# Optimization experiments

Measured on AMD Instinct MI355X. Metric: run time of the kernel, lower is better.

Reference implementation:

```python
import jax, jax.numpy as jnp
import numpy as np

MA_K = 25  # moving-average window for temporal pattern decoupling (trend extraction)
BN_EPS = 1e-5


def conv1d(x, w, b, dilation=1, padding=0, groups=1):
    # x: [N, C, L], w: [O, I/groups, K]
    out = jax.lax.conv_general_dilated(
        x, w, window_strides=(1,), padding=[(padding, padding)],
        rhs_dilation=(dilation,), dimension_numbers=("NCH", "OIH", "NCH"),
        feature_group_count=groups)
    if b is not None:
        out = out + b[None, :, None]
    return out


def moving_avg(x):
    # series-decomposition trend: depthwise uniform conv with edge padding
    c = x.shape[1]
    xp = jnp.pad(x, ((0, 0), (0, 0), (MA_K // 2, MA_K // 2)), mode="edge")
    k = jnp.full((c, 1, MA_K), 1.0 / MA_K, dtype=x.dtype)
    return conv1d(xp, k, None, dilation=1, padding=0, groups=c)


def setup_inputs() -> dict:
    key = jax.random.key(0)
    ks = jax.random.split(key, 12)
    B, C, L = 16, 256, 4096
    nb = 4
    c = C // nb  # 64 per branch
    inp = {
        "x": jax.random.normal(ks[0], (B, C, L), dtype=jnp.float32),
        # stacked per-branch Conv1dBlock params (all branches share c)
        "conv_w": jax.random.normal(ks[1], (nb, c, c, 3), dtype=jnp.float32) * 0.05,
        "conv_b": jax.random.normal(ks[2], (nb, c), dtype=jnp.float32) * 0.05,
        "bn_gamma": 1.0 + 0.1 * jax.random.normal(ks[3], (nb, c), dtype=jnp.float32),
        "bn_beta": 0.1 * jax.random.normal(ks[4], (nb, c), dtype=jnp.float32),
        "bn_mean": 0.1 * jax.random.normal(ks[5], (nb, c), dtype=jnp.float32),
        "bn_var": 0.5 + jax.random.uniform(ks[6], (nb, c), dtype=jnp.float32),
        # fusion 1x1 conv: 2C -> C
        "fusion_w": jax.random.normal(ks[7], (C, 2 * C, 1), dtype=jnp.float32) * 0.02,
        "fusion_b": jax.random.normal(ks[8], (C,), dtype=jnp.float32) * 0.02,
        "alpha": jnp.ones((1,), dtype=jnp.float32),
    }
    return inp


def reference(x, conv_w, conv_b, bn_gamma, bn_beta, bn_mean, bn_var,
              fusion_w, fusion_b, alpha):
    nb = conv_w.shape[0]
    parts = jnp.split(x, nb, axis=1)  # equal branch channels (C % nb == 0)
    shorts, longs = [], []
    for i in range(nb):
        d = 2 ** i  # dilation; padding = d keeps length for k=3
        h = conv1d(parts[i], conv_w[i], conv_b[i], dilation=d, padding=d)
        # BatchNorm1d, inference semantics (running stats)
        inv = jax.lax.rsqrt(bn_var[i] + BN_EPS)
        h = (h - bn_mean[i][None, :, None]) * (bn_gamma[i] * inv)[None, :, None] \
            + bn_beta[i][None, :, None]
        h = jax.nn.gelu(h, approximate=False)
        # TemporalPatternDecoupling: long = moving-average trend, short = residual
        l = moving_avg(h)
        s = h - l
        # dim_check AdaptiveAvgPool1d(seq_len) and F.interpolate(size=L) are
        # identity here since every branch already has length L == seq_len
        shorts.append(s)
        longs.append(l)
    # cumulative fuse: short forward, long backward
    for b in range(1, nb):
        shorts[b] = shorts[b] + shorts[b - 1]
    for b in reversed(range(nb - 1)):
        longs[b] = longs[b] + longs[b + 1]
    fused = jnp.concatenate(shorts + longs, axis=1)  # [B, 2C, L]
    out = jax.nn.relu(conv1d(fused, fusion_w, fusion_b))
    return out + alpha[0] * x
```

## Files before the change

### kernel.cpp

```cpp
#include <hip/hip_runtime.h>
#include <math.h>

#define BATCH 16
#define CCH 256
#define LSEQ 4096
#define NB 4
#define CB 64
#define MA_H 12
#define BN_EPS 1e-5f

typedef __attribute__((ext_vector_type(8))) short bf16x8;
typedef __attribute__((ext_vector_type(4))) float f32x4;

__device__ inline float b2f(ushort u) {
    union { uint i; float f; } v; v.i = ((uint)u) << 16; return v.f;
}
__device__ inline ushort f2b(float f) {
    uint x = __float_as_uint(f);
    return (ushort)((x + 0x7FFFu + ((x >> 16) & 1u)) >> 16);
}
__device__ inline float gelu_fast(float v) {
    float t2 = fmaf(0.044715f, v * v, 1.f);
    float u2 = 1.59576912160573f * v * t2;
    float e  = __expf(u2);
    float r  = __frcp_rn(e + 1.f);
    return v * (1.f - r);
}

__global__ __launch_bounds__(256) void k0w_fusionw(const float* __restrict__ fw,
                                                   ushort* __restrict__ wbf2)
{
    int e = blockIdx.x * 256 + threadIdx.x;
    int o = e >> 6, j = e & 63;
    const float* row = fw + (size_t)o * 512;
    float ws0 = row[j],       ws1 = row[64 + j],
          ws2 = row[128 + j], ws3 = row[192 + j];
    float wl0 = row[256 + j], wl1 = row[320 + j],
          wl2 = row[384 + j], wl3 = row[448 + j];
    float S3 = ws3, S2 = ws2 + S3, S1 = ws1 + S2, S0 = ws0 + S1;
    float L0 = wl0, L1 = L0 + wl1, L2 = L1 + wl2, L3 = L2 + wl3;
    ushort* dst = wbf2 + (size_t)o * 512;
    dst[j]        = f2b(S0); dst[64 + j]  = f2b(S1);
    dst[128 + j]  = f2b(S2); dst[192 + j] = f2b(S3);
    dst[256 + j]  = f2b(L0 - S0); dst[320 + j] = f2b(L1 - S1);
    dst[384 + j]  = f2b(L2 - S2); dst[448 + j] = f2b(L3 - S3);
}

__global__ __launch_bounds__(256) void k0b_convw_branch(
    const float* __restrict__ conv_w, ushort* __restrict__ wbr)
{
    int e = blockIdx.x * 256 + threadIdx.x;
    int i    = e & 63;
    int rest = e >> 6;
    int kk   = rest % 3;
    int orow = rest / 3;
    float v = conv_w[(size_t)orow * 192 + i * 3 + kk];
    wbr[(size_t)orow * 192 + kk * 64 + i] = f2b(v);
}

__global__ __launch_bounds__(256) void k0c_xT(const float* __restrict__ x,
                                              ushort* __restrict__ xT)
{
    const int p0    = blockIdx.x * 64;
    const int batch = blockIdx.y;
    const int tid   = threadIdx.x;

    __shared__ uint ls[256 * 33];

    const float* xb = x + (size_t)batch * CCH * LSEQ;
#pragma unroll
    for (int pass = 0; pass < 16; ++pass) {
        int e  = tid + pass * 256;
        int ch = e >> 4;
        int c4 = e & 15;
        float4 v = *(const float4*)&xb[(size_t)ch * LSEQ + p0 + c4 * 4];
        uint u0 = (uint)f2b(v.x) | ((uint)f2b(v.y) << 16);
        uint u1 = (uint)f2b(v.z) | ((uint)f2b(v.w) << 16);
        ls[ch * 33 + c4 * 2]     = u0;
        ls[ch * 33 + c4 * 2 + 1] = u1;
    }
    __syncthreads();

    const int w = tid >> 6, l = tid & 63;
    const ushort* lsu = (const ushort*)ls;
    ushort* dst = xT + ((size_t)batch * LSEQ + p0) * CCH;
#pragma unroll
    for (int r = 0; r < 16; ++r) {
        int p = w * 16 + r;
#pragma unroll
        for (int q = 0; q < 4; ++q) {
            int ch = l + 64 * q;
            dst[(size_t)p * CCH + ch] = lsu[ch * 66 + p];
        }
    }
}

#define SXA 72
#define SWB 200
#define K1T 2
__global__ __launch_bounds__(256) void k1_conv_mfma(
    const ushort* __restrict__ xT, const ushort* __restrict__ wbr,
    const float* __restrict__ conv_b, const float* __restrict__ bn_gamma,
    const float* __restrict__ bn_beta, const float* __restrict__ bn_mean,
    const float* __restrict__ bn_var, ushort* __restrict__ hT)
{
    const int br    = blockIdx.y;
    const int batch = blockIdx.z;
    const int d     = 1 << br;
    const int tid   = threadIdx.x;
    const int wm    = tid >> 6;
    const int lane  = tid & 63;
    const int lo    = lane & 15;
    const int hi    = lane >> 4;

    __shared__ ushort xsA[144 * SXA];
    __shared__ ushort wlB[64 * SWB];

    const ushort* xTb = xT + (size_t)batch * LSEQ * CCH + br * CB;

    {
        const ushort* wrow = wbr + ((size_t)br * CB) * 192;
#pragma unroll
        for (int pass = 0; pass < 6; ++pass) {
            int e = tid + pass * 256;
            int o = e / 24;
            int c = e - o * 24;
            uint4 v = *(const uint4*)&wrow[e * 8];
            *(uint4*)&wlB[o * SWB + c * 8] = v;
        }
    }
    float bias[4], sc[4], sh[4];
#pragma unroll
    for (int ni = 0; ni < 4; ++ni) {
        const int go = br * CB + ni * 16 + lo;
        bias[ni] = conv_b[go];
        float inv = rsqrtf(bn_var[go] + BN_EPS);
        sc[ni] = bn_gamma[go] * inv;
        sh[ni] = bn_beta[go] - bn_mean[go] * sc[ni];
    }

    const int arow = tid >> 3;
    const int acol = tid & 7;
    uint4 areg[5];
    {
        const int t0 = blockIdx.x * (K1T * 128);
#pragma unroll
        for (int pass = 0; pass < 5; ++pass) {
            int p = arow + pass * 32;
            areg[pass] = make_uint4(0u, 0u, 0u, 0u);
            if (p < 144) {
                int gp = t0 - 8 + p;
                if (gp >= 0 && gp < LSEQ)
                    areg[pass] = *(const uint4*)&xTb[(size_t)gp * CCH + acol * 8];
            }
        }
    }

    for (int t = 0; t < K1T; ++t) {
        const int t0 = blockIdx.x * (K1T * 128) + t * 128;
        __syncthreads();
#pragma unroll
        for (int pass = 0; pass < 5; ++pass) {
            int p = arow + pass * 32;
            if (p < 144) *(uint4*)&xsA[p * SXA + acol * 8] = areg[pass];
        }
        __syncthreads();

        f32x4 acc[2][4];
#pragma unroll
        for (int mi = 0; mi < 2; ++mi)
#pragma unroll
            for (int ni = 0; ni < 4; ++ni) acc[mi][ni] = (f32x4)0.f;

#pragma unroll
        for (int kk = 0; kk < 3; ++kk) {
            const int roff = 8 + (kk - 1) * d;
#pragma unroll
            for (int ks = 0; ks < 2; ++ks) {
                bf16x8 af[2], bfr[4];
#pragma unroll
                for (int mi = 0; mi < 2; ++mi)
                    af[mi] = *(const bf16x8*)&xsA[
                        (wm * 32 + mi * 16 + lo + roff) * SXA + ks * 32 + hi * 8];
#pragma unroll
                for (int ni = 0; ni < 4; ++ni)
                    bfr[ni] = *(const bf16x8*)&wlB[
                        (ni * 16 + lo) * SWB + kk * 64 + ks * 32 + hi * 8];
#pragma unroll
                for (int mi = 0; mi < 2; ++mi)
#pragma unroll
                    for (int ni = 0; ni < 4; ++ni)
                        acc[mi][ni] = __builtin_amdgcn_mfma_f32_16x16x32_bf16(
                            af[mi], bfr[ni], acc[mi][ni], 0, 0, 0);
            }
        }

        if (t + 1 < K1T) {
            const int tn = t0 + 128;
#pragma unroll
            for (int pass = 0; pass < 5; ++pass) {
                int p = arow + pass * 32;
                areg[pass] = make_uint4(0u, 0u, 0u, 0u);
                if (p < 144) {
                    int gp = tn - 8 + p;
                    if (gp >= 0 && gp < LSEQ)
                        areg[pass] = *(const uint4*)&xTb[(size_t)gp * CCH + acol * 8];
                }
            }
        }

        __syncthreads();
        ushort* os = xsA;
#pragma unroll
        for (int ni = 0; ni < 4; ++ni) {
            const int o = ni * 16 + lo;
#pragma unroll
            for (int mi = 0; mi < 2; ++mi) {
                const int prow = wm * 32 + mi * 16 + hi * 4;
#pragma unroll
                for (int q = 0; q < 4; ++q) {
                    float v = acc[mi][ni][q] + bias[ni];
                    v = v * sc[ni] + sh[ni];
                    os[(prow + q) * SXA + o] = f2b(gelu_fast(v));
                }
            }
        }
        __syncthreads();
        ushort* hTb = hT + ((size_t)batch * LSEQ + t0) * CCH + br * CB;
#pragma unroll
        for (int pass = 0; pass < 4; ++pass) {
            int e = tid + pass * 256;
            int r = e >> 3;
            int c = e & 7;
            *(uint4*)&hTb[(size_t)r * CCH + c * 8] = *(const uint4*)&xsA[r * SXA + c * 8];
        }
    }
}

#define LS_S 68
__global__ __launch_bounds__(256) void k2_ma(
    const ushort* __restrict__ hT, ushort* __restrict__ hmaT)
{
    const int p0    = blockIdx.x * 128;
    const int cg    = blockIdx.y;
    const int batch = blockIdx.z;
    const int tid   = threadIdx.x;

    __shared__ ushort ls[152 * LS_S];
    __shared__ ushort os[128 * LS_S];

    const ushort* src = hT + ((size_t)batch * LSEQ) * CCH + cg * 64;
#pragma unroll
    for (int pass = 0; pass < 10; ++pass) {
        int e = tid + pass * 256;
        int r = e >> 4;
        int c = e & 15;
        if (r < 152) {
            int gp = p0 - MA_H + r;
            gp = max(0, min(LSEQ - 1, gp));
            *(uint2*)&ls[r * LS_S + c * 4] = *(const uint2*)&src[(size_t)gp * CCH + c * 4];
        }
    }
    __syncthreads();

    const int ch = tid & 63;
    const int pg = tid >> 6;
    const int r0 = pg * 32;
    const float inv25 = 1.f / 25.f;

    float s = 0.f;
#pragma unroll
    for (int t = 0; t < 25; ++t) s += b2f(ls[(r0 + t) * LS_S + ch]);
    os[(r0 + 0) * LS_S + ch] = f2b(s * inv25);
#pragma unroll
    for (int t = 1; t < 32; ++t) {
        s += b2f(ls[(r0 + 24 + t) * LS_S + ch]) - b2f(ls[(r0 + t - 1) * LS_S + ch]);
        os[(r0 + t) * LS_S + ch] = f2b(s * inv25);
    }
    __syncthreads();

    ushort* dst = hmaT + ((size_t)batch * LSEQ + p0) * CCH + cg * 64;
#pragma unroll
    for (int pass = 0; pass < 8; ++pass) {
        int e = tid + pass * 256;
        int r = e >> 4;
        int c = e & 15;
        *(uint2*)&dst[(size_t)r * CCH + c * 4] = *(const uint2*)&os[r * LS_S + c * 4];
    }
}

#define KTOT 512
#define SA 72
__global__ __launch_bounds__(256) void k3_fusion(
    const ushort* __restrict__ hT, const ushort* __restrict__ hmaT,
    const ushort* __restrict__ wbf2, const float* __restrict__ fb,
    const float* __restrict__ x, const float* __restrict__ alpha,
    float* __restrict__ out)
{
    const int t0    = blockIdx.x * 128;
    const int oBase = blockIdx.y * 128;
    const int batch = blockIdx.z;
    const int tid   = threadIdx.x;
    const int wid   = tid >> 6;
    const int lane  = tid & 63;
    const int lo    = lane & 15;
    const int hi    = lane >> 4;
    const int wm    = wid >> 1;
    const int wn    = wid & 1;

    __shared__ short AL[128 * SA];
    __shared__ short WL[128 * SA];

    f32x4 acc[4][4];
#pragma unroll
    for (int mi = 0; mi < 4; ++mi)
#pragma unroll
        for (int ni = 0; ni < 4; ++ni) acc[mi][ni] = (f32x4)0.f;

    const int srow = tid >> 3;
    const int scol = tid & 7;

    for (int k0 = 0; k0 < KTOT; k0 += 64) {
        const ushort* asrc = (k0 < 256)
            ? hT   + ((size_t)(batch * LSEQ + t0)) * CCH + k0
            : hmaT + ((size_t)(batch * LSEQ + t0)) * CCH + (k0 - 256);
        __syncthreads();
#pragma unroll
        for (int pass = 0; pass < 4; ++pass) {
            int row = pass * 32 + srow;
            uint4 va = *(const uint4*)&asrc[(size_t)row * CCH + scol * 8];
            *(uint4*)&AL[row * SA + scol * 8] = va;
            uint4 vw = *(const uint4*)&wbf2[
                (size_t)(oBase + row) * KTOT + k0 + scol * 8];
            *(uint4*)&WL[row * SA + scol * 8] = vw;
        }
        __syncthreads();

#pragma unroll
        for (int ks = 0; ks < 2; ++ks) {
            bf16x8 af[4], bfr[4];
#pragma unroll
            for (int mi = 0; mi < 4; ++mi)
                af[mi] = *(const bf16x8*)&AL[(wm * 64 + mi * 16 + lo) * SA + ks * 32 + hi * 8];
#pragma unroll
            for (int ni = 0; ni < 4; ++ni)
                bfr[ni] = *(const bf16x8*)&WL[(wn * 64 + ni * 16 + lo) * SA + ks * 32 + hi * 8];
#pragma unroll
            for (int mi = 0; mi < 4; ++mi)
#pragma unroll
                for (int ni = 0; ni < 4; ++ni)
                    acc[mi][ni] = __builtin_amdgcn_mfma_f32_16x16x32_bf16(
                        af[mi], bfr[ni], acc[mi][ni], 0, 0, 0);
        }
    }

    const float al = alpha[0];
#pragma unroll
    for (int ni = 0; ni < 4; ++ni) {
        const int o = oBase + wn * 64 + ni * 16 + lo;
        const float bias = fb[o];
#pragma unroll
        for (int mi = 0; mi < 4; ++mi) {
            const int pos = t0 + wm * 64 + mi * 16 + hi * 4;
            size_t base = ((size_t)(batch * CCH + o)) * LSEQ + pos;
            float4 xv = *(const float4*)&x[base];
            float4 ov;
            ov.x = fmaxf(acc[mi][ni][0] + bias, 0.f) + al * xv.x;
            ov.y = fmaxf(acc[mi][ni][1] + bias, 0.f) + al * xv.y;
            ov.z = fmaxf(acc[mi][ni][2] + bias, 0.f) + al * xv.z;
            ov.w = fmaxf(acc[mi][ni][3] + bias, 0.f) + al * xv.w;
            *(float4*)&out[base] = ov;
        }
    }
}

extern "C" void kernel_launch(void* const* d_in, const int* in_sizes, int n_in,
                              void* d_out, int out_size, void* d_ws, size_t ws_size,
                              hipStream_t stream)
{
    const float* x        = (const float*)d_in[0];
    const float* conv_w   = (const float*)d_in[1];
    const float* conv_b   = (const float*)d_in[2];
    const float* bn_gamma = (const float*)d_in[3];
    const float* bn_beta  = (const float*)d_in[4];
    const float* bn_mean  = (const float*)d_in[5];
    const float* bn_var   = (const float*)d_in[6];
    const float* fw       = (const float*)d_in[7];
    const float* fb       = (const float*)d_in[8];
    const float* alpha    = (const float*)d_in[9];
    float* out = (float*)d_out;

    ushort* hT    = (ushort*)d_ws;
    ushort* hmaT  = (ushort*)((char*)d_ws + (size_t)32 * 1024 * 1024);
    ushort* wbf2  = (ushort*)((char*)d_ws + (size_t)96 * 1024 * 1024);
    ushort* wbr   = (ushort*)((char*)d_ws + (size_t)97 * 1024 * 1024);
    ushort* xT    = (ushort*)((char*)d_ws + (size_t)98 * 1024 * 1024);

    k0w_fusionw<<<dim3(64), 256, 0, stream>>>(fw, wbf2);
    k0b_convw_branch<<<dim3(192), 256, 0, stream>>>(conv_w, wbr);
    k0c_xT<<<dim3(64, 16), 256, 0, stream>>>(x, xT);

    dim3 g1(16, NB, BATCH);
    k1_conv_mfma<<<g1, 256, 0, stream>>>(xT, wbr, conv_b, bn_gamma, bn_beta,
                                         bn_mean, bn_var, hT);
    dim3 g2(32, 4, BATCH);
    k2_ma<<<g2, 256, 0, stream>>>(hT, hmaT);

    dim3 g3(32, 2, BATCH);
    k3_fusion<<<g3, 256, 0, stream>>>(hT, hmaT, wbf2, fb, x, alpha, out);
}
```

Baseline: 104.9 us.

## Double-buffer fusion GEMM activations with direct global-to-LDS loads and swizzle

```diff
diff --git a/kernel.cpp b/kernel.cpp
--- a/kernel.cpp
+++ b/kernel.cpp
@@ -25,6 +25,11 @@
     float e  = __expf(u2);
     float r  = __frcp_rn(e + 1.f);
     return v * (1.f - r);
+}
+__device__ __forceinline__ void gload_lds16(const void* g, void* l) {
+    __builtin_amdgcn_global_load_lds(
+        (const __attribute__((address_space(1))) void*)g,
+        (__attribute__((address_space(3))) void*)l, 16, 0, 0);
 }
 
 __global__ __launch_bounds__(256) void k0w_fusionw(const float* __restrict__ fw,
@@ -290,7 +295,6 @@
 }
 
 #define KTOT 512
-#define SA 72
 __global__ __launch_bounds__(256) void k3_fusion(
     const ushort* __restrict__ hT, const ushort* __restrict__ hmaT,
     const ushort* __restrict__ wbf2, const float* __restrict__ fb,
@@ -308,8 +312,7 @@
     const int wm    = wid >> 1;
     const int wn    = wid & 1;
 
-    __shared__ short AL[128 * SA];
-    __shared__ short WL[128 * SA];
+    __shared__ __align__(16) ushort AL2[2][128 * 64];
 
     f32x4 acc[4][4];
 #pragma unroll
@@ -317,34 +320,47 @@
 #pragma unroll
         for (int ni = 0; ni < 4; ++ni) acc[mi][ni] = (f32x4)0.f;
 
-    const int srow = tid >> 3;
-    const int scol = tid & 7;
-
+    const ushort* hTb   = hT   + ((size_t)(batch * LSEQ + t0)) * CCH;
+    const ushort* hmaTb = hmaT + ((size_t)(batch * LSEQ + t0)) * CCH;
+
+    const int srow0 = lane >> 3;
+    const int scc   = lane & 7;
+
+#define K3_STAGE(buf, kn)                                                     \
+    {                                                                         \
+        const ushort* asrc = ((kn) < 256) ? (hTb + (kn))                      \
+                                          : (hmaTb + ((kn) - 256));           \
+        _Pragma("unroll")                                                     \
+        for (int i = 0; i < 4; ++i) {                                         \
+            int s = wid * 4 + i;                                              \
+            int r = s * 8 + srow0;                                            \
+            int q = scc ^ (r & 7);                                            \
+            gload_lds16(asrc + (size_t)r * CCH + q * 8,                       \
+                        (char*)&AL2[buf][0] + s * 1024);                      \
+        }                                                                     \
+    }
+
+    K3_STAGE(0, 0);
+    __syncthreads();
+
+    int cur = 0;
     for (int k0 = 0; k0 < KTOT; k0 += 64) {
-        const ushort* asrc = (k0 < 256)
-            ? hT   + ((size_t)(batch * LSEQ + t0)) * CCH + k0
-            : hmaT + ((size_t)(batch * LSEQ + t0)) * CCH + (k0 - 256);
-        __syncthreads();
-#pragma unroll
-        for (int pass = 0; pass < 4; ++pass) {
-            int row = pass * 32 + srow;
-            uint4 va = *(const uint4*)&asrc[(size_t)row * CCH + scol * 8];
-            *(uint4*)&AL[row * SA + scol * 8] = va;
-            uint4 vw = *(const uint4*)&wbf2[
-                (size_t)(oBase + row) * KTOT + k0 + scol * 8];
-            *(uint4*)&WL[row * SA + scol * 8] = vw;
-        }
-        __syncthreads();
+        if (k0 + 64 < KTOT) K3_STAGE(cur ^ 1, k0 + 64);
 
 #pragma unroll
         for (int ks = 0; ks < 2; ++ks) {
             bf16x8 af[4], bfr[4];
 #pragma unroll
-            for (int mi = 0; mi < 4; ++mi)
-                af[mi] = *(const bf16x8*)&AL[(wm * 64 + mi * 16 + lo) * SA + ks * 32 + hi * 8];
+            for (int mi = 0; mi < 4; ++mi) {
+                int row = wm * 64 + mi * 16 + lo;
+                int cc = (ks * 4 + hi) ^ (row & 7);
+                af[mi] = *(const bf16x8*)&AL2[cur][row * 64 + cc * 8];
+            }
 #pragma unroll
             for (int ni = 0; ni < 4; ++ni)
-                bfr[ni] = *(const bf16x8*)&WL[(wn * 64 + ni * 16 + lo) * SA + ks * 32 + hi * 8];
+                bfr[ni] = *(const bf16x8*)&wbf2[
+                    (size_t)(oBase + wn * 64 + ni * 16 + lo) * KTOT
+                    + k0 + ks * 32 + hi * 8];
 #pragma unroll
             for (int mi = 0; mi < 4; ++mi)
 #pragma unroll
@@ -352,6 +368,8 @@
                     acc[mi][ni] = __builtin_amdgcn_mfma_f32_16x16x32_bf16(
                         af[mi], bfr[ni], acc[mi][ni], 0, 0, 0);
         }
+        __syncthreads();
+        cur ^= 1;
     }
 
     const float al = alpha[0];
```

Result: slower. 129.9 us (+23.8%).

## Fold moving average into fusion GEMM by commuting it past the linear projection

Applied to the files above, without the earlier changes.

```diff
diff --git a/kernel.cpp b/kernel.cpp
--- a/kernel.cpp
+++ b/kernel.cpp
@@ -237,138 +237,145 @@
     }
 }
 
-#define LS_S 68
-__global__ __launch_bounds__(256) void k2_ma(
-    const ushort* __restrict__ hT, ushort* __restrict__ hmaT)
-{
-    const int p0    = blockIdx.x * 128;
-    const int cg    = blockIdx.y;
-    const int batch = blockIdx.z;
-    const int tid   = threadIdx.x;
-
-    __shared__ ushort ls[152 * LS_S];
-    __shared__ ushort os[128 * LS_S];
-
-    const ushort* src = hT + ((size_t)batch * LSEQ) * CCH + cg * 64;
-#pragma unroll
-    for (int pass = 0; pass < 10; ++pass) {
-        int e = tid + pass * 256;
-        int r = e >> 4;
-        int c = e & 15;
-        if (r < 152) {
-            int gp = p0 - MA_H + r;
-            gp = max(0, min(LSEQ - 1, gp));
-            *(uint2*)&ls[r * LS_S + c * 4] = *(const uint2*)&src[(size_t)gp * CCH + c * 4];
-        }
-    }
-    __syncthreads();
-
-    const int ch = tid & 63;
-    const int pg = tid >> 6;
-    const int r0 = pg * 32;
-    const float inv25 = 1.f / 25.f;
-
-    float s = 0.f;
-#pragma unroll
-    for (int t = 0; t < 25; ++t) s += b2f(ls[(r0 + t) * LS_S + ch]);
-    os[(r0 + 0) * LS_S + ch] = f2b(s * inv25);
-#pragma unroll
-    for (int t = 1; t < 32; ++t) {
-        s += b2f(ls[(r0 + 24 + t) * LS_S + ch]) - b2f(ls[(r0 + t - 1) * LS_S + ch]);
-        os[(r0 + t) * LS_S + ch] = f2b(s * inv25);
-    }
-    __syncthreads();
-
-    ushort* dst = hmaT + ((size_t)batch * LSEQ + p0) * CCH + cg * 64;
-#pragma unroll
-    for (int pass = 0; pass < 8; ++pass) {
-        int e = tid + pass * 256;
-        int r = e >> 4;
-        int c = e & 15;
-        *(uint2*)&dst[(size_t)r * CCH + c * 4] = *(const uint2*)&os[r * LS_S + c * 4];
-    }
-}
-
-#define KTOT 512
-#define SA 72
-__global__ __launch_bounds__(256) void k3_fusion(
-    const ushort* __restrict__ hT, const ushort* __restrict__ hmaT,
-    const ushort* __restrict__ wbf2, const float* __restrict__ fb,
-    const float* __restrict__ x, const float* __restrict__ alpha,
-    float* __restrict__ out)
+__global__ __launch_bounds__(256) void k3_fused(
+    const ushort* __restrict__ hT, const ushort* __restrict__ wbf2,
+    const float* __restrict__ fb, const float* __restrict__ x,
+    const float* __restrict__ alpha, float* __restrict__ out)
 {
     const int t0    = blockIdx.x * 128;
-    const int oBase = blockIdx.y * 128;
+    const int oBase = blockIdx.y * 64;
     const int batch = blockIdx.z;
     const int tid   = threadIdx.x;
     const int wid   = tid >> 6;
     const int lane  = tid & 63;
     const int lo    = lane & 15;
     const int hi    = lane >> 4;
-    const int wm    = wid >> 1;
-    const int wn    = wid & 1;
-
-    __shared__ short AL[128 * SA];
-    __shared__ short WL[128 * SA];
-
-    f32x4 acc[4][4];
-#pragma unroll
-    for (int mi = 0; mi < 4; ++mi)
-#pragma unroll
-        for (int ni = 0; ni < 4; ++ni) acc[mi][ni] = (f32x4)0.f;
-
-    const int srow = tid >> 3;
-    const int scol = tid & 7;
-
-    for (int k0 = 0; k0 < KTOT; k0 += 64) {
-        const ushort* asrc = (k0 < 256)
-            ? hT   + ((size_t)(batch * LSEQ + t0)) * CCH + k0
-            : hmaT + ((size_t)(batch * LSEQ + t0)) * CCH + (k0 - 256);
-        __syncthreads();
-#pragma unroll
-        for (int pass = 0; pass < 4; ++pass) {
-            int row = pass * 32 + srow;
-            uint4 va = *(const uint4*)&asrc[(size_t)row * CCH + scol * 8];
-            *(uint4*)&AL[row * SA + scol * 8] = va;
-            uint4 vw = *(const uint4*)&wbf2[
-                (size_t)(oBase + row) * KTOT + k0 + scol * 8];
-            *(uint4*)&WL[row * SA + scol * 8] = vw;
+
+    __shared__ __align__(16) ushort SMEM[23040];
+    ushort* A_s  = SMEM;
+    ushort* WS_s = SMEM + 13824;
+    ushort* WL_s = SMEM + 18432;
+    ushort* G_l  = SMEM;
+    ushort* M_l  = SMEM + 13824;
+
+    f32x4 accS[2][4];
+    f32x4 accG[3][4];
+#pragma unroll
+    for (int a = 0; a < 2; ++a)
+#pragma unroll
+        for (int b = 0; b < 4; ++b) accS[a][b] = (f32x4)0.f;
+#pragma unroll
+    for (int a = 0; a < 3; ++a)
+#pragma unroll
+        for (int b = 0; b < 4; ++b) accG[a][b] = (f32x4)0.f;
+
+    const ushort* hTb = hT + ((size_t)batch * LSEQ) * CCH;
+
+    for (int kn = 0; kn < 4; ++kn) {
+        __syncthreads();
+#pragma unroll
+        for (int pass = 0; pass < 6; ++pass) {
+            int e = tid + pass * 256;
+            int r = e >> 3;
+            int c = e & 7;
+            int gp = t0 - 32 + r;
+            gp = max(0, min(LSEQ - 1, gp));
+            *(uint4*)&A_s[r * 72 + c * 8] =
+                *(const uint4*)&hTb[(size_t)gp * CCH + kn * 64 + c * 8];
+        }
+#pragma unroll
+        for (int pass = 0; pass < 2; ++pass) {
+            int e = tid + pass * 256;
+            int r = e >> 3;
+            int c = e & 7;
+            const ushort* wrow = wbf2 + (size_t)(oBase + r) * 512;
+            *(uint4*)&WS_s[r * 72 + c * 8] = *(const uint4*)&wrow[kn * 64 + c * 8];
+            *(uint4*)&WL_s[r * 72 + c * 8] = *(const uint4*)&wrow[256 + kn * 64 + c * 8];
         }
         __syncthreads();
 
 #pragma unroll
         for (int ks = 0; ks < 2; ++ks) {
-            bf16x8 af[4], bfr[4];
-#pragma unroll
-            for (int mi = 0; mi < 4; ++mi)
-                af[mi] = *(const bf16x8*)&AL[(wm * 64 + mi * 16 + lo) * SA + ks * 32 + hi * 8];
-#pragma unroll
-            for (int ni = 0; ni < 4; ++ni)
-                bfr[ni] = *(const bf16x8*)&WL[(wn * 64 + ni * 16 + lo) * SA + ks * 32 + hi * 8];
-#pragma unroll
-            for (int mi = 0; mi < 4; ++mi)
+            bf16x8 afS[2], afG[3], bS[4], bL[4];
+#pragma unroll
+            for (int mi = 0; mi < 2; ++mi)
+                afS[mi] = *(const bf16x8*)&A_s[
+                    (32 + wid * 32 + mi * 16 + lo) * 72 + ks * 32 + hi * 8];
+#pragma unroll
+            for (int j = 0; j < 3; ++j)
+                afG[j] = *(const bf16x8*)&A_s[
+                    (wid * 48 + j * 16 + lo) * 72 + ks * 32 + hi * 8];
+#pragma unroll
+            for (int ni = 0; ni < 4; ++ni) {
+                bS[ni] = *(const bf16x8*)&WS_s[
+                    (ni * 16 + lo) * 72 + ks * 32 + hi * 8];
+                bL[ni] = *(const bf16x8*)&WL_s[
+                    (ni * 16 + lo) * 72 + ks * 32 + hi * 8];
+            }
+#pragma unroll
+            for (int mi = 0; mi < 2; ++mi)
 #pragma unroll
                 for (int ni = 0; ni < 4; ++ni)
-                    acc[mi][ni] = __builtin_amdgcn_mfma_f32_16x16x32_bf16(
-                        af[mi], bfr[ni], acc[mi][ni], 0, 0, 0);
-        }
-    }
+                    accS[mi][ni] = __builtin_amdgcn_mfma_f32_16x16x32_bf16(
+                        afS[mi], bS[ni], accS[mi][ni], 0, 0, 0);
+#pragma unroll
+            for (int j = 0; j < 3; ++j)
+#pragma unroll
+                for (int ni = 0; ni < 4; ++ni)
+                    accG[j][ni] = __builtin_amdgcn_mfma_f32_16x16x32_bf16(
+                        afG[j], bL[ni], accG[j][ni], 0, 0, 0);
+        }
+    }
+    __syncthreads();
+
+#pragma unroll
+    for (int j = 0; j < 3; ++j)
+#pragma unroll
+        for (int ni = 0; ni < 4; ++ni) {
+            int o    = ni * 16 + lo;
+            int grow = wid * 48 + j * 16 + hi * 4;
+            ushort4 gv;
+            gv.x = f2b(accG[j][ni][0]); gv.y = f2b(accG[j][ni][1]);
+            gv.z = f2b(accG[j][ni][2]); gv.w = f2b(accG[j][ni][3]);
+            *(ushort4*)&G_l[o * 196 + grow] = gv;
+        }
+    __syncthreads();
+
+    {
+        const int o  = tid & 63;
+        const int p0 = (tid >> 6) * 32;
+        const int ob = o * 196;
+        const float inv25 = 1.f / 25.f;
+        float s = 0.f;
+#pragma unroll
+        for (int r = 20; r <= 44; ++r) s += b2f(G_l[ob + p0 + r]);
+        M_l[o * 132 + p0] = f2b(s * inv25);
+#pragma unroll 4
+        for (int t = 1; t < 32; ++t) {
+            s += b2f(G_l[ob + p0 + t + 44]) - b2f(G_l[ob + p0 + t + 19]);
+            M_l[o * 132 + p0 + t] = f2b(s * inv25);
+        }
+    }
+    __syncthreads();
 
     const float al = alpha[0];
 #pragma unroll
     for (int ni = 0; ni < 4; ++ni) {
-        const int o = oBase + wn * 64 + ni * 16 + lo;
+        const int ol = ni * 16 + lo;
+        const int o  = oBase + ol;
         const float bias = fb[o];
 #pragma unroll
-        for (int mi = 0; mi < 4; ++mi) {
-            const int pos = t0 + wm * 64 + mi * 16 + hi * 4;
+        for (int mi = 0; mi < 2; ++mi) {
+            const int pl  = wid * 32 + mi * 16 + hi * 4;
+            const int pos = t0 + pl;
+            ushort4 m4 = *(const ushort4*)&M_l[ol * 132 + pl];
             size_t base = ((size_t)(batch * CCH + o)) * LSEQ + pos;
             float4 xv = *(const float4*)&x[base];
             float4 ov;
-            ov.x = fmaxf(acc[mi][ni][0] + bias, 0.f) + al * xv.x;
-            ov.y = fmaxf(acc[mi][ni][1] + bias, 0.f) + al * xv.y;
-            ov.z = fmaxf(acc[mi][ni][2] + bias, 0.f) + al * xv.z;
-            ov.w = fmaxf(acc[mi][ni][3] + bias, 0.f) + al * xv.w;
+            ov.x = fmaxf(accS[mi][ni][0] + b2f(m4.x) + bias, 0.f) + al * xv.x;
+            ov.y = fmaxf(accS[mi][ni][1] + b2f(m4.y) + bias, 0.f) + al * xv.y;
+            ov.z = fmaxf(accS[mi][ni][2] + b2f(m4.z) + bias, 0.f) + al * xv.z;
+            ov.w = fmaxf(accS[mi][ni][3] + b2f(m4.w) + bias, 0.f) + al * xv.w;
             *(float4*)&out[base] = ov;
         }
     }
@@ -391,7 +398,6 @@
     float* out = (float*)d_out;
 
     ushort* hT    = (ushort*)d_ws;
-    ushort* hmaT  = (ushort*)((char*)d_ws + (size_t)32 * 1024 * 1024);
     ushort* wbf2  = (ushort*)((char*)d_ws + (size_t)96 * 1024 * 1024);
     ushort* wbr   = (ushort*)((char*)d_ws + (size_t)97 * 1024 * 1024);
     ushort* xT    = (ushort*)((char*)d_ws + (size_t)98 * 1024 * 1024);
@@ -403,9 +409,7 @@
     dim3 g1(16, NB, BATCH);
     k1_conv_mfma<<<g1, 256, 0, stream>>>(xT, wbr, conv_b, bn_gamma, bn_beta,
                                          bn_mean, bn_var, hT);
-    dim3 g2(32, 4, BATCH);
-    k2_ma<<<g2, 256, 0, stream>>>(hT, hmaT);
-
-    dim3 g3(32, 2, BATCH);
-    k3_fusion<<<g3, 256, 0, stream>>>(hT, hmaT, wbf2, fb, x, alpha, out);
-}
+
+    dim3 g3(32, 4, BATCH);
+    k3_fused<<<g3, 256, 0, stream>>>(hT, wbf2, fb, x, alpha, out);
+}
```

After: 132.7 us. 26.5% more time.
